# Kernel tuning notes

Hardware: AMD Instinct MI355X
Metric: run time of the kernel (lower is better)

Reference implementation:

```python
import jax, jax.numpy as jnp
import numpy as np

B, S, I, H, O, L = 32, 512, 1024, 1024, 1024, 2
W_SCALE = 0.03  # keep gate pre-activations in a sane range


def setup_inputs() -> dict:
    key = jax.random.key(0)
    ks = jax.random.split(key, 10)
    rn = lambda k, shape: jax.random.normal(k, shape, dtype=jnp.float32)
    return {
        "x": rn(ks[0], (B, S, I)),
        "h0": jnp.zeros((L, B, H), jnp.float32),
        "Wxz": rn(ks[1], (L, H, H)) * W_SCALE,
        "Wxr": rn(ks[2], (L, H, H)) * W_SCALE,
        "Wxg": rn(ks[3], (L, H, H)) * W_SCALE,
        "Whz": rn(ks[4], (L, H, H)) * W_SCALE,
        "Whr": rn(ks[5], (L, H, H)) * W_SCALE,
        "Whg": rn(ks[6], (L, H, H)) * W_SCALE,
        "bhz": jnp.zeros((L, H), jnp.float32),
        "bhr": jnp.zeros((L, H), jnp.float32),
        "bhg": jnp.zeros((L, H), jnp.float32),
        "WY": rn(ks[7], (O, H)) * W_SCALE,
        "bY": jnp.zeros((O,), jnp.float32),
    }


def reference(x, h0, Wxz, Wxr, Wxg, Whz, Whr, Whg, bhz, bhr, bhg, WY, bY):
    # x: [B,S,I]; h0: [L,B,H]. PyTorch Linear: y = x @ W.T (+ b).
    def step(h, x_t):            # h: [L,B,H], x_t: [B,I]
        xk = x_t
        new_h = []
        for k in range(L):       # static small layer loop
            hk = h[k]
            z = jax.nn.sigmoid(xk @ Wxz[k].T + hk @ Whz[k].T + bhz[k])
            r = jax.nn.sigmoid(xk @ Wxr[k].T + hk @ Whr[k].T + bhr[k])
            g = jnp.tanh(xk @ Wxg[k].T + (r * hk) @ Whg[k].T + bhg[k])
            hk = z * hk + (1.0 - z) * g
            new_h.append(hk)
            xk = hk              # dropout=0 -> identity
        y_t = xk @ WY.T + bY     # [B,O]
        return jnp.stack(new_h), y_t

    h_final, ys = jax.lax.scan(step, h0, jnp.swapaxes(x, 0, 1))  # ys: [S,B,O]
    layer_output = jnp.swapaxes(ys, 0, 1)                         # [B,S,O]
    hidden_state = jnp.swapaxes(h_final, 0, 1)                    # [B,L,H]
    return layer_output, hidden_state
```

## Files before the change

### kernel.cpp

```cpp
#include <hip/hip_runtime.h>
#include <hip/hip_bf16.h>

typedef __bf16 bf16x8 __attribute__((ext_vector_type(8)));
typedef float floatx4 __attribute__((ext_vector_type(4)));

#define HID 1024
#define HH (1024*1024)
#define SEQ 512
#define NB 32768
#define NBLK 256

__device__ __forceinline__ float bf2f(unsigned short u) {
  union { unsigned int i; float f; } v; v.i = ((unsigned int)u) << 16; return v.f;
}
__device__ __forceinline__ unsigned short f2bf(float f) {
  union { float f; unsigned int i; } v; v.f = f;
  unsigned int i = v.i;
  return (unsigned short)((i + 0x7fffu + ((i >> 16) & 1u)) >> 16);
}
__device__ __forceinline__ float ldflag(const void* p, long i, int flag) {
  return flag ? ((const float*)p)[i] : bf2f(((const unsigned short*)p)[i]);
}
__device__ __forceinline__ float sigmoidf_(float x) { return 1.0f / (1.0f + __expf(-x)); }

#define GSTH(p_, v_)   asm volatile("global_store_short %0, %1, off sc0 sc1" :: "v"(p_), "v"(v_) : "memory")
#define GSTW(p_, v_)   asm volatile("global_store_dword %0, %1, off sc0 sc1" :: "v"(p_), "v"(v_) : "memory")

__device__ __forceinline__ void outw_wt(void* out, int flag, long idx, float v) {
  if (flag) { GSTW((float*)out + idx, v); }
  else      { GSTH((unsigned short*)out + idx, (unsigned int)f2bf(v)); }
}

__global__ void detect_k(const unsigned int* __restrict__ xw, int* __restrict__ flag) {
  unsigned int w = xw[threadIdx.x];
  int e = (w >> 7) & 0xFF;
  int ok = (e >= 100 && e <= 141) ? 1 : 0;
  unsigned long long m = __ballot(ok);
  if (threadIdx.x == 0) *flag = (__popcll(m) >= 36) ? 0 : 1;
}

__global__ void convert_k(const float* __restrict__ x,
                          const float* __restrict__ w0, const float* __restrict__ w1,
                          const float* __restrict__ w2, const float* __restrict__ w3,
                          const float* __restrict__ w4, const float* __restrict__ w5,
                          const float* __restrict__ wy,
                          unsigned short* __restrict__ xb, unsigned short* __restrict__ wc,
                          unsigned short* __restrict__ wyc, const int* __restrict__ flag) {
  if (*flag == 0) return;
  const float* Ws[6] = { w0, w1, w2, w3, w4, w5 };
  const long total = 3801088;
  for (long c = (long)blockIdx.x * 256 + threadIdx.x; c < total; c += (long)gridDim.x * 256) {
    long e = c * 8;
    const float* src; unsigned short* dst; long off;
    if (e < 16777216)      { src = x;  dst = xb;  off = e; }
    else if (e < 29360128) { long r = e - 16777216; int wi = (int)(r >> 21);
                             src = Ws[wi]; dst = wc + (long)wi * 2097152; off = r & 2097151; }
    else                   { src = wy; dst = wyc; off = e - 29360128; }
    float4 a = *(const float4*)(src + off);
    float4 b = *(const float4*)(src + off + 4);
    uint4 o;
    o.x = (unsigned)f2bf(a.x) | ((unsigned)f2bf(a.y) << 16);
    o.y = (unsigned)f2bf(a.z) | ((unsigned)f2bf(a.w) << 16);
    o.z = (unsigned)f2bf(b.x) | ((unsigned)f2bf(b.y) << 16);
    o.w = (unsigned)f2bf(b.z) | ((unsigned)f2bf(b.w) << 16);
    *(uint4*)(dst + off) = o;
  }
}

__device__ __forceinline__ void gbar(int* cnt, int target, int blk) {
  __syncthreads();
  if (threadIdx.x == 0) {
    __builtin_amdgcn_fence(__ATOMIC_RELEASE, "agent");
    __hip_atomic_fetch_add(cnt + (blk & 7) * 64, 1, __ATOMIC_RELAXED, __HIP_MEMORY_SCOPE_AGENT);
    int ssum;
    do {
      ssum = 0;
      #pragma unroll
      for (int i = 0; i < 8; ++i)
        ssum += __hip_atomic_load(cnt + i * 64, __ATOMIC_RELAXED, __HIP_MEMORY_SCOPE_AGENT);
      if (ssum < target) __builtin_amdgcn_s_sleep(1);
    } while (ssum < target);
    __builtin_amdgcn_fence(__ATOMIC_ACQUIRE, "agent");
  }
  __syncthreads();
}

__device__ __forceinline__ void gbar7(int* xcdArr, int* gTot, int* xcdGo,
                                      int myxcd, int xcdTot, int lead, int pidx) {
  asm volatile("s_waitcnt vmcnt(0)" ::: "memory");
  __syncthreads();
  if (threadIdx.x == 0) {
    int old = __hip_atomic_fetch_add(xcdArr + myxcd * 64, 1,
                                     __ATOMIC_RELAXED, __HIP_MEMORY_SCOPE_AGENT);
    if (old == pidx * xcdTot - 1) {
      __builtin_amdgcn_fence(__ATOMIC_RELEASE, "agent");
      __hip_atomic_fetch_add(gTot, xcdTot, __ATOMIC_RELAXED, __HIP_MEMORY_SCOPE_AGENT);
    }
    if (lead) {
      while (__hip_atomic_load(gTot, __ATOMIC_RELAXED, __HIP_MEMORY_SCOPE_AGENT)
             < NBLK * pidx)
        __builtin_amdgcn_s_sleep(1);
      __builtin_amdgcn_fence(__ATOMIC_ACQUIRE, "agent");
      __hip_atomic_store(xcdGo + myxcd * 64, pidx,
                         __ATOMIC_RELAXED, __HIP_MEMORY_SCOPE_AGENT);
    } else {
      asm volatile("buffer_inv" ::: "memory");
      while (__hip_atomic_load(xcdGo + myxcd * 64, __ATOMIC_RELAXED,
                               __HIP_MEMORY_SCOPE_AGENT) < pidx)
        __builtin_amdgcn_s_sleep(1);
    }
  }
  __syncthreads();
}

__device__ __forceinline__ void stage2(unsigned short* dst,
                                       const unsigned short* __restrict__ s0,
                                       const unsigned short* __restrict__ s1,
                                       int n0, int tid) {
  const unsigned short* srcs[2] = { s0, s1 };
  #pragma unroll
  for (int i = 0; i < 16; ++i) {
    int idx = i * 256 + tid;
    int m = idx >> 11;
    int rem = idx & 2047;
    int r = rem >> 7, k8 = rem & 127;
    bf16x8 v = *(const bf16x8*)(srcs[m] + (long)(n0 + r) * HID + k8 * 8);
    int kc = k8 >> 2, L = ((k8 & 3) << 4) | r;
    *(bf16x8*)(dst + (((m * 32 + kc) * 64 + L) << 3)) = v;
  }
}
__device__ __forceinline__ void stage1(unsigned short* dst,
                                       const unsigned short* __restrict__ s0,
                                       int n0, int tid) {
  #pragma unroll
  for (int i = 0; i < 8; ++i) {
    int idx = i * 256 + tid;
    int r = idx >> 7, k8 = idx & 127;
    bf16x8 v = *(const bf16x8*)(s0 + (long)(n0 + r) * HID + k8 * 8);
    int kc = k8 >> 2, L = ((k8 & 3) << 4) | r;
    *(bf16x8*)(dst + ((kc * 64 + L) << 3)) = v;
  }
}

__device__ __forceinline__ floatx4 gpair(const unsigned short* __restrict__ a1,
                                         const unsigned short* __restrict__ a2,
                                         const unsigned short* sW, int khalf, int lane) {
  floatx4 acc = {0.f, 0.f, 0.f, 0.f};
  const unsigned short* w1 = sW + (((khalf * 16) * 64 + lane) << 3);
  const unsigned short* w2 = sW + (((32 + khalf * 16) * 64 + lane) << 3);
  #pragma unroll
  for (int j = 0; j < 16; ++j)
    acc = __builtin_amdgcn_mfma_f32_16x16x32_bf16(*(const bf16x8*)(a1 + j * 32),
                                                  *(const bf16x8*)(w1 + j * 512), acc, 0, 0, 0);
  #pragma unroll
  for (int j = 0; j < 16; ++j)
    acc = __builtin_amdgcn_mfma_f32_16x16x32_bf16(*(const bf16x8*)(a2 + j * 32),
                                                  *(const bf16x8*)(w2 + j * 512), acc, 0, 0, 0);
  return acc;
}
__device__ __forceinline__ floatx4 gsingle(const unsigned short* __restrict__ a,
                                           const unsigned short* sW, int khalf, int lane) {
  floatx4 acc = {0.f, 0.f, 0.f, 0.f};
  const unsigned short* w = sW + (((khalf * 16) * 64 + lane) << 3);
  #pragma unroll
  for (int j = 0; j < 16; ++j)
    acc = __builtin_amdgcn_mfma_f32_16x16x32_bf16(*(const bf16x8*)(a + j * 32),
                                                  *(const bf16x8*)(w + j * 512), acc, 0, 0, 0);
  return acc;
}

__global__ void __launch_bounds__(256, 1) gru2(
    const void* __restrict__ x, const void* __restrict__ h0i,
    const void* __restrict__ Wxz, const void* __restrict__ Wxr, const void* __restrict__ Wxg,
    const void* __restrict__ Whz, const void* __restrict__ Whr, const void* __restrict__ Whg,
    const void* __restrict__ bhz, const void* __restrict__ bhr, const void* __restrict__ bhg,
    const void* __restrict__ WY, const void* __restrict__ bY,
    void* __restrict__ out, const int* __restrict__ flagp, int* __restrict__ barBase,
    const unsigned short* __restrict__ xb, const unsigned short* __restrict__ wcv,
    const unsigned short* __restrict__ wyc,
    float* __restrict__ h0f, float* __restrict__ h1f,
    float* __restrict__ z0f, float* __restrict__ z1f,
    unsigned short* __restrict__ h0b, unsigned short* __restrict__ h1b,
    unsigned short* __restrict__ rh0, unsigned short* __restrict__ rh1)
{
  extern __shared__ char smem[];
  unsigned short* sWP = (unsigned short*)smem;
  unsigned short* sWQ = (unsigned short*)(smem + 65536);
  floatx4* red = (floatx4*)(smem + 131072);

  int* barCnt   = barBase;
  int* xcdArr   = barBase + 512;
  int* gTot     = barBase + 1024;
  int* xcdGo    = barBase + 2048;
  int* xcdCount = barBase + 2560;

  const int flag = *flagp;
  const int thr  = threadIdx.x;
  const int wave = thr >> 6;
  const int lane = thr & 63;
  const int l15  = lane & 15;
  const int kq   = (lane >> 4) * 8;
  const int blk  = blockIdx.x;
  const int role = blk >> 6;
  const int c0   = (blk & 63) * 16;
  const int myxcd = __builtin_amdgcn_s_getreg(20 | (3 << 11)) & 7;

  const unsigned short* xP  = flag ? xb                : (const unsigned short*)x;
  const unsigned short* Wzp = flag ? wcv + 0L*2097152  : (const unsigned short*)Wxz;
  const unsigned short* Wrp = flag ? wcv + 1L*2097152  : (const unsigned short*)Wxr;
  const unsigned short* Wgp = flag ? wcv + 2L*2097152  : (const unsigned short*)Wxg;
  const unsigned short* Uzp = flag ? wcv + 3L*2097152  : (const unsigned short*)Whz;
  const unsigned short* Urp = flag ? wcv + 4L*2097152  : (const unsigned short*)Whr;
  const unsigned short* Ugp = flag ? wcv + 5L*2097152  : (const unsigned short*)Whg;
  const unsigned short* WYp = flag ? wyc               : (const unsigned short*)WY;

  int lead = 0;
  if (thr == 0) {
    int old = __hip_atomic_fetch_add(xcdCount + myxcd * 64, 1,
                                     __ATOMIC_RELAXED, __HIP_MEMORY_SCOPE_AGENT);
    lead = (old == 0);
  }

  {
    long off = (role >> 1) ? (long)HH : 0;
    const unsigned short* s0 = ((role & 1) ? Wrp : Wzp) + off;
    const unsigned short* s1 = ((role & 1) ? Urp : Uzp) + off;
    stage2(sWP, s0, s1, c0, thr);
  }
  if (blk < 128)      stage2(sWQ, Wgp + (blk >= 64 ? (long)HH : 0),
                             Ugp + (blk >= 64 ? (long)HH : 0), c0, thr);
  else if (blk < 192) stage1(sWQ, WYp, (blk - 128) * 16, thr);

  {
    int gtid = blk * 256 + thr;
    int layer = gtid >> 15, i = gtid & 32767;
    float v = ldflag(h0i, (long)layer * NB + i, flag);
    unsigned int b = f2bf(v);
    if (layer == 0) { GSTW(h0f + i, v); GSTH(h0b + i, b); GSTH(h0b + NB + i, b); }
    else            { GSTW(h1f + i, v); GSTH(h1b + i, b); GSTH(h1b + NB + i, b); }
  }
  asm volatile("s_waitcnt vmcnt(0)" ::: "memory");
  gbar(barCnt, NBLK, blk);

  int xcdTot = 0;
  if (thr == 0)
    xcdTot = __hip_atomic_load(xcdCount + myxcd * 64, __ATOMIC_RELAXED, __HIP_MEMORY_SCOPE_AGENT);
  int pidx = 0;

  for (int s = 0; s < SEQ + 2; ++s) {
    const int pPrev  = ((s + 1) & 1) * NB;
    const int pPrev2 = (s & 1) * NB;
    const int mt = wave & 1, khalf = wave >> 1;
    const int m = mt * 16 + l15;
    const int aoff = kq + khalf * 512;

    {
      const int layer = role >> 1, zr = role & 1;
      const bool active = layer ? (s >= 1 && s <= SEQ) : (s < SEQ);
      if (active) {
        const unsigned short *a1, *a2;
        if (layer == 0) {
          a1 = xP + (long)m * (SEQ * HID) + (long)s * HID + aoff;
          a2 = h0b + pPrev + m * HID + aoff;
        } else {
          a1 = h0b + pPrev + m * HID + aoff;
          a2 = h1b + pPrev2 + m * HID + aoff;
        }
        floatx4 acc = gpair(a1, a2, sWP, khalf, lane);
        red[wave * 64 + lane] = acc;
        __syncthreads();
        if (wave < 2) {
          floatx4 ss = red[wave * 64 + lane] + red[(wave + 2) * 64 + lane];
          int n = c0 + l15;
          float bv = ldflag(zr ? bhr : bhz, (long)layer * HID + n, flag);
          #pragma unroll
          for (int r = 0; r < 4; ++r) {
            int row = wave * 16 + (lane >> 4) * 4 + r;
            int idx = row * HID + n;
            float v = sigmoidf_(ss[r] + bv);
            if (role == 0)      GSTW(z0f + idx, v);
            else if (role == 1) GSTH(rh0 + idx, (unsigned int)f2bf(v * h0f[idx]));
            else if (role == 2) GSTW(z1f + idx, v);
            else                GSTH(rh1 + idx, (unsigned int)f2bf(v * h1f[idx]));
          }
        }
      }
    }
    ++pidx; gbar7(xcdArr, gTot, xcdGo, myxcd, xcdTot, lead, pidx);

    if (role == 0) {
      if (s < SEQ) {
        const unsigned short* a1 = xP + (long)m * (SEQ * HID) + (long)s * HID + aoff;
        const unsigned short* a2 = rh0 + m * HID + aoff;
        floatx4 acc = gpair(a1, a2, sWQ, khalf, lane);
        red[wave * 64 + lane] = acc;
        __syncthreads();
        if (wave < 2) {
          floatx4 ss = red[wave * 64 + lane] + red[(wave + 2) * 64 + lane];
          int n = c0 + l15;
          float bv = ldflag(bhg, n, flag);
          #pragma unroll
          for (int r = 0; r < 4; ++r) {
            int row = wave * 16 + (lane >> 4) * 4 + r;
            int idx = row * HID + n;
            float g = tanhf(ss[r] + bv);
            float z = z0f[idx], hp = h0f[idx];
            float hn = z * hp + (1.f - z) * g;
            GSTW(h0f + idx, hn);
            GSTH(h0b + (s & 1) * NB + idx, (unsigned int)f2bf(hn));
            if (s == SEQ - 1) outw_wt(out, flag, 16777216L + (long)row * 2048 + n, hn);
          }
        }
      }
    } else if (role == 1) {
      if (s >= 1 && s <= SEQ) {
        const unsigned short* a1 = h0b + pPrev + m * HID + aoff;
        const unsigned short* a2 = rh1 + m * HID + aoff;
        floatx4 acc = gpair(a1, a2, sWQ, khalf, lane);
        red[wave * 64 + lane] = acc;
        __syncthreads();
        if (wave < 2) {
          floatx4 ss = red[wave * 64 + lane] + red[(wave + 2) * 64 + lane];
          int n = c0 + l15;
          float bv = ldflag(bhg, (long)HID + n, flag);
          #pragma unroll
          for (int r = 0; r < 4; ++r) {
            int row = wave * 16 + (lane >> 4) * 4 + r;
            int idx = row * HID + n;
            float g = tanhf(ss[r] + bv);
            float z = z1f[idx], hp = h1f[idx];
            float hn = z * hp + (1.f - z) * g;
            GSTW(h1f + idx, hn);
            GSTH(h1b + ((s + 1) & 1) * NB + idx, (unsigned int)f2bf(hn));
            if (s == SEQ) outw_wt(out, flag, 16777216L + (long)row * 2048 + 1024 + n, hn);
          }
        }
      }
    } else if (role == 2) {
      if (s >= 2) {
        const int cy = (blk - 128) * 16;
        const unsigned short* a = h1b + pPrev2 + m * HID + aoff;
        floatx4 acc = gsingle(a, sWQ, khalf, lane);
        red[wave * 64 + lane] = acc;
        __syncthreads();
        if (wave < 2) {
          floatx4 ss = red[wave * 64 + lane] + red[(wave + 2) * 64 + lane];
          int n = cy + l15;
          float bv = ldflag(bY, n, flag);
          const int tY = s - 2;
          #pragma unroll
          for (int r = 0; r < 4; ++r) {
            int brow = wave * 16 + (lane >> 4) * 4 + r;
            long oidx = ((long)brow * SEQ + tY) * HID + n;
            outw_wt(out, flag, oidx, ss[r] + bv);
          }
        }
      }
    }
    ++pidx; gbar7(xcdArr, gTot, xcdGo, myxcd, xcdTot, lead, pidx);
  }
}

extern "C" void kernel_launch(void* const* d_in, const int* in_sizes, int n_in,
                              void* d_out, int out_size, void* d_ws, size_t ws_size,
                              hipStream_t stream) {
  const void* x   = d_in[0];
  const void* h0i = d_in[1];
  const void* Wxz = d_in[2];
  const void* Wxr = d_in[3];
  const void* Wxg = d_in[4];
  const void* Whz = d_in[5];
  const void* Whr = d_in[6];
  const void* Whg = d_in[7];
  const void* bhz = d_in[8];
  const void* bhr = d_in[9];
  const void* bhg = d_in[10];
  const void* WY  = d_in[11];
  const void* bY  = d_in[12];

  char* ws = (char*)d_ws;
  int* flag    = (int*)ws;
  int* barBase = (int*)(ws + 1024);
  float* h0f = (float*)(ws + 16384);
  float* h1f = h0f + NB;
  float* z0f = h1f + NB;
  float* z1f = z0f + NB;
  unsigned short* h0b = (unsigned short*)(z1f + NB);
  unsigned short* h1b = h0b + 2 * NB;
  unsigned short* rh0 = h1b + 2 * NB;
  unsigned short* rh1 = rh0 + NB;
  unsigned short* xb  = (unsigned short*)(ws + (1 << 20));
  unsigned short* wcv = xb + 16777216L;
  unsigned short* wyc = wcv + 12582912L;

  hipMemsetAsync(barBase, 0, 12288, stream);
  detect_k<<<1, 64, 0, stream>>>((const unsigned int*)x, flag);
  convert_k<<<2048, 256, 0, stream>>>((const float*)x,
      (const float*)Wxz, (const float*)Wxr, (const float*)Wxg,
      (const float*)Whz, (const float*)Whr, (const float*)Whg,
      (const float*)WY, xb, wcv, wyc, flag);

  static int attr_set = 0;
  if (!attr_set) {
    hipFuncSetAttribute((const void*)gru2, hipFuncAttributeMaxDynamicSharedMemorySize, 135168);
    attr_set = 1;
  }

  void* out = d_out;
  const int* flagc = flag;
  int* barc = barBase;
  void* args[] = { (void*)&x, (void*)&h0i, (void*)&Wxz, (void*)&Wxr, (void*)&Wxg,
                   (void*)&Whz, (void*)&Whr, (void*)&Whg, (void*)&bhz, (void*)&bhr,
                   (void*)&bhg, (void*)&WY, (void*)&bY, (void*)&out, (void*)&flagc,
                   (void*)&barc, (void*)&xb, (void*)&wcv, (void*)&wyc,
                   (void*)&h0f, (void*)&h1f, (void*)&z0f, (void*)&z1f,
                   (void*)&h0b, (void*)&h1b, (void*)&rh0, (void*)&rh1 };
  hipLaunchCooperativeKernel((const void*)gru2, dim3(NBLK), dim3(256), args, 135168, stream);
}
```

Measured before the change: 8.649 ms.

## Use four-slot ring buffers for GRU state and relax per-barrier acquire fences

```diff
diff --git a/kernel.cpp b/kernel.cpp
--- a/kernel.cpp
+++ b/kernel.cpp
@@ -9,6 +9,7 @@
 #define SEQ 512
 #define NB 32768
 #define NBLK 256
+#define SL(k) ((((k) & 3)) * NB)
 
 __device__ __forceinline__ float bf2f(unsigned short u) {
   union { unsigned int i; float f; } v; v.i = ((unsigned int)u) << 16; return v.f;
@@ -85,7 +86,7 @@
   __syncthreads();
 }
 
-__device__ __forceinline__ void gbar7(int* xcdArr, int* gTot, int* xcdGo,
+__device__ __forceinline__ void gbar8(int* xcdArr, int* gTot, int* xcdGo,
                                       int myxcd, int xcdTot, int lead, int pidx) {
   asm volatile("s_waitcnt vmcnt(0)" ::: "memory");
   __syncthreads();
@@ -100,7 +101,10 @@
       while (__hip_atomic_load(gTot, __ATOMIC_RELAXED, __HIP_MEMORY_SCOPE_AGENT)
              < NBLK * pidx)
         __builtin_amdgcn_s_sleep(1);
-      __builtin_amdgcn_fence(__ATOMIC_ACQUIRE, "agent");
+      if ((pidx & 3) == 0)
+        __builtin_amdgcn_fence(__ATOMIC_ACQUIRE, "agent");
+      else
+        asm volatile("buffer_inv" ::: "memory");
       __hip_atomic_store(xcdGo + myxcd * 64, pidx,
                          __ATOMIC_RELAXED, __HIP_MEMORY_SCOPE_AGENT);
     } else {
@@ -236,8 +240,8 @@
     int layer = gtid >> 15, i = gtid & 32767;
     float v = ldflag(h0i, (long)layer * NB + i, flag);
     unsigned int b = f2bf(v);
-    if (layer == 0) { GSTW(h0f + i, v); GSTH(h0b + i, b); GSTH(h0b + NB + i, b); }
-    else            { GSTW(h1f + i, v); GSTH(h1b + i, b); GSTH(h1b + NB + i, b); }
+    if (layer == 0) { GSTW(h0f + SL(3) + i, v); GSTH(h0b + SL(3) + i, b); }
+    else            { GSTW(h1f + SL(3) + i, v); GSTH(h1b + SL(3) + i, b); }
   }
   asm volatile("s_waitcnt vmcnt(0)" ::: "memory");
   gbar(barCnt, NBLK, blk);
@@ -248,8 +252,9 @@
   int pidx = 0;
 
   for (int s = 0; s < SEQ + 2; ++s) {
-    const int pPrev  = ((s + 1) & 1) * NB;
-    const int pPrev2 = (s & 1) * NB;
+    const int sCur   = SL(s);
+    const int sPrev  = SL(s - 1);
+    const int sPrev2 = SL(s - 2);
     const int mt = wave & 1, khalf = wave >> 1;
     const int m = mt * 16 + l15;
     const int aoff = kq + khalf * 512;
@@ -261,10 +266,10 @@
         const unsigned short *a1, *a2;
         if (layer == 0) {
           a1 = xP + (long)m * (SEQ * HID) + (long)s * HID + aoff;
-          a2 = h0b + pPrev + m * HID + aoff;
+          a2 = h0b + sPrev + m * HID + aoff;
         } else {
-          a1 = h0b + pPrev + m * HID + aoff;
-          a2 = h1b + pPrev2 + m * HID + aoff;
+          a1 = h0b + sPrev + m * HID + aoff;
+          a2 = h1b + sPrev2 + m * HID + aoff;
         }
         floatx4 acc = gpair(a1, a2, sWP, khalf, lane);
         red[wave * 64 + lane] = acc;
@@ -279,19 +284,21 @@
             int idx = row * HID + n;
             float v = sigmoidf_(ss[r] + bv);
             if (role == 0)      GSTW(z0f + idx, v);
-            else if (role == 1) GSTH(rh0 + idx, (unsigned int)f2bf(v * h0f[idx]));
-            else if (role == 2) GSTW(z1f + idx, v);
-            else                GSTH(rh1 + idx, (unsigned int)f2bf(v * h1f[idx]));
+            else if (role == 1) GSTH(rh0 + sCur + idx,
+                                     (unsigned int)f2bf(v * h0f[sPrev + idx]));
+            else if (role == 2) GSTW(z1f + sCur + idx, v);
+            else                GSTH(rh1 + sCur + idx,
+                                     (unsigned int)f2bf(v * h1f[sPrev2 + idx]));
           }
         }
       }
     }
-    ++pidx; gbar7(xcdArr, gTot, xcdGo, myxcd, xcdTot, lead, pidx);
+    ++pidx; gbar8(xcdArr, gTot, xcdGo, myxcd, xcdTot, lead, pidx);
 
     if (role == 0) {
       if (s < SEQ) {
         const unsigned short* a1 = xP + (long)m * (SEQ * HID) + (long)s * HID + aoff;
-        const unsigned short* a2 = rh0 + m * HID + aoff;
+        const unsigned short* a2 = rh0 + sCur + m * HID + aoff;
         floatx4 acc = gpair(a1, a2, sWQ, khalf, lane);
         red[wave * 64 + lane] = acc;
         __syncthreads();
@@ -304,18 +311,18 @@
             int row = wave * 16 + (lane >> 4) * 4 + r;
             int idx = row * HID + n;
             float g = tanhf(ss[r] + bv);
-            float z = z0f[idx], hp = h0f[idx];
+            float z = z0f[idx], hp = h0f[sPrev + idx];
             float hn = z * hp + (1.f - z) * g;
-            GSTW(h0f + idx, hn);
-            GSTH(h0b + (s & 1) * NB + idx, (unsigned int)f2bf(hn));
+            GSTW(h0f + sCur + idx, hn);
+            GSTH(h0b + sCur + idx, (unsigned int)f2bf(hn));
             if (s == SEQ - 1) outw_wt(out, flag, 16777216L + (long)row * 2048 + n, hn);
           }
         }
       }
     } else if (role == 1) {
       if (s >= 1 && s <= SEQ) {
-        const unsigned short* a1 = h0b + pPrev + m * HID + aoff;
-        const unsigned short* a2 = rh1 + m * HID + aoff;
+        const unsigned short* a1 = h0b + sPrev + m * HID + aoff;
+        const unsigned short* a2 = rh1 + sCur + m * HID + aoff;
         floatx4 acc = gpair(a1, a2, sWQ, khalf, lane);
         red[wave * 64 + lane] = acc;
         __syncthreads();
@@ -328,10 +335,10 @@
             int row = wave * 16 + (lane >> 4) * 4 + r;
             int idx = row * HID + n;
             float g = tanhf(ss[r] + bv);
-            float z = z1f[idx], hp = h1f[idx];
+            float z = z1f[sCur + idx], hp = h1f[sPrev2 + idx];
             float hn = z * hp + (1.f - z) * g;
-            GSTW(h1f + idx, hn);
-            GSTH(h1b + ((s + 1) & 1) * NB + idx, (unsigned int)f2bf(hn));
+            GSTW(h1f + sPrev + idx, hn);
+            GSTH(h1b + sPrev + idx, (unsigned int)f2bf(hn));
             if (s == SEQ) outw_wt(out, flag, 16777216L + (long)row * 2048 + 1024 + n, hn);
           }
         }
@@ -339,7 +346,7 @@
     } else if (role == 2) {
       if (s >= 2) {
         const int cy = (blk - 128) * 16;
-        const unsigned short* a = h1b + pPrev2 + m * HID + aoff;
+        const unsigned short* a = h1b + sPrev2 + m * HID + aoff;
         floatx4 acc = gsingle(a, sWQ, khalf, lane);
         red[wave * 64 + lane] = acc;
         __syncthreads();
@@ -357,7 +364,7 @@
         }
       }
     }
-    ++pidx; gbar7(xcdArr, gTot, xcdGo, myxcd, xcdTot, lead, pidx);
+    ++pidx; gbar8(xcdArr, gTot, xcdGo, myxcd, xcdTot, lead, pidx);
   }
 }
 
@@ -381,15 +388,15 @@
   char* ws = (char*)d_ws;
   int* flag    = (int*)ws;
   int* barBase = (int*)(ws + 1024);
-  float* h0f = (float*)(ws + 16384);
-  float* h1f = h0f + NB;
-  float* z0f = h1f + NB;
-  float* z1f = z0f + NB;
-  unsigned short* h0b = (unsigned short*)(z1f + NB);
-  unsigned short* h1b = h0b + 2 * NB;
-  unsigned short* rh0 = h1b + 2 * NB;
-  unsigned short* rh1 = rh0 + NB;
-  unsigned short* xb  = (unsigned short*)(ws + (1 << 20));
+  float* z0f = (float*)(ws + 16384);
+  float* h0f = z0f + NB;
+  float* h1f = h0f + 4 * NB;
+  float* z1f = h1f + 4 * NB;
+  unsigned short* h0b = (unsigned short*)(z1f + 4 * NB);
+  unsigned short* h1b = h0b + 4 * NB;
+  unsigned short* rh0 = h1b + 4 * NB;
+  unsigned short* rh1 = rh0 + 4 * NB;
+  unsigned short* xb  = (unsigned short*)(ws + 3145728);
   unsigned short* wcv = xb + 16777216L;
   unsigned short* wyc = wcv + 12582912L;
 
```

Measured after the change: 8.615 ms. No clear change (-0.4%).
